# Kernel optimization log

Measured on AMD Instinct MI355X. Metric: run time of the kernel, lower is better.

The kernel has to match this reference:

```python
import jax, jax.numpy as jnp
import numpy as np

B, S, ENC = 64, 2048, 1024          # batch, encoder seq len, encoder feature dim
U, E_DIM, V_SZ = 512, 256, 50000    # dec_units, embedding_dim, vocab_size
IN_DIM = ENC + E_DIM                # LSTM input: [context ; token embedding]


def setup_inputs() -> dict:
    key = jax.random.key(0)
    ks = jax.random.split(key, 16)
    g = lambda k, shp, s=0.02: (jax.random.normal(k, shp, jnp.float32) * s)
    return {
        "x": jax.random.randint(ks[0], (B, 1), 0, V_SZ),
        "c_fwd": g(ks[1], (B, U), 0.1),
        "c_bwd": g(ks[2], (B, U), 0.1),
        "enc_output": jax.random.normal(ks[3], (B, S, ENC), jnp.float32),
        "emb": g(ks[4], (V_SZ, E_DIM)),
        "W1_w": g(ks[5], (ENC, U)), "W1_b": jnp.zeros((U,), jnp.float32),
        "W2_w": g(ks[6], (U, U)),   "W2_b": jnp.zeros((U,), jnp.float32),
        "W3_w": g(ks[7], (U, U)),   "W3_b": jnp.zeros((U,), jnp.float32),
        "V_w": g(ks[8], (U, 1)),    "V_b": jnp.zeros((1,), jnp.float32),
        "Kf": g(ks[9], (IN_DIM, 4 * U)),  "bf": jnp.zeros((4 * U,), jnp.float32),
        "Kb": g(ks[10], (IN_DIM, 4 * U)), "bb": jnp.zeros((4 * U,), jnp.float32),
        "fc_w": g(ks[11], (2 * U, V_SZ)), "fc_b": jnp.zeros((V_SZ,), jnp.float32),
    }


def _lstm_step_zero_state(xin, K, b):
    # Keras LSTM single step from zero (h0, c0): recurrent term vanishes.
    # Gate order in Keras kernel: i, f, c(g), o.
    z = xin @ K + b
    i, f, g, o = jnp.split(z, 4, axis=-1)
    i, o = jax.nn.sigmoid(i), jax.nn.sigmoid(o)  # f gate multiplies c0=0
    c = i * jnp.tanh(g)
    h = o * jnp.tanh(c)
    return h, c


def reference(x, c_fwd, c_bwd, enc_output, emb,
              W1_w, W1_b, W2_w, W2_b, W3_w, W3_b, V_w, V_b,
              Kf, bf, Kb, bb, fc_w, fc_b):
    # Bahdanau additive attention: score [B, S, 1]
    hidden_proj = (c_fwd @ W2_w + W2_b + c_bwd @ W3_w + W3_b)[:, None, :]  # [B,1,U]
    score = jnp.tanh(enc_output @ W1_w + W1_b + hidden_proj) @ V_w + V_b
    attn = jax.nn.softmax(score, axis=1)                 # softmax over S
    ctx = jnp.sum(attn * enc_output, axis=1)             # [B, ENC]

    xe = emb[x[:, 0]]                                    # [B, E_DIM]
    xin = jnp.concatenate([ctx, xe], axis=-1)            # [B, ENC+E_DIM]

    # Bidirectional LSTM over a length-1 sequence from zero initial state:
    # both directions see the same single timestep with separate weights.
    hf, cf = _lstm_step_zero_state(xin, Kf, bf)
    hb, cb = _lstm_step_zero_state(xin, Kb, bb)

    out = jnp.concatenate([hf, hb], axis=-1)             # [B, 2U]
    logits = out @ fc_w + fc_b                           # [B, vocab]
    return logits, hf, cf, hb, cb
```

## Files before the change

kernel.cpp:

```cpp
#include <hip/hip_runtime.h>

using u16 = unsigned short;
typedef float f32x4 __attribute__((ext_vector_type(4)));
typedef __bf16 bf16x8 __attribute__((ext_vector_type(8)));
typedef u16 u16x8 __attribute__((ext_vector_type(8)));

static constexpr int OF_HPB   = 262144;
static constexpr int OF_CTXP  = 294912;
static constexpr int OF_STATS = 2392064;
static constexpr int OF_XIN   = 2394112;
static constexpr int OF_ZPART = 2476032;
static constexpr size_t SCRATCH_FLOATS = 3000320;
static constexpr size_t SCRATCH_BYTES = SCRATCH_FLOATS * 4ull;

__device__ __forceinline__ u16 f2bf(float f) {
  unsigned u = __float_as_uint(f);
  u += 0x7FFFu + ((u >> 16) & 1u);
  return (u16)(u >> 16);
}
__device__ __forceinline__ float fast_tanh(float x) {
  x = fminf(fmaxf(x, -20.f), 20.f);
  float e = __expf(2.f * x);
  return (e - 1.f) / (e + 1.f);
}
__device__ __forceinline__ float fast_sig(float x) { return 1.f / (1.f + __expf(-x)); }

__global__ void k_prep_w1(const float* __restrict__ W1w, u16* __restrict__ w1p) {
  __shared__ float tile[32][132];
  const int t = threadIdx.x;
  const int ks = blockIdx.x >> 2, u0 = (blockIdx.x & 3) * 128;
  {
    int kk = t >> 3, ui = (t & 7) * 16;
    const float* src = W1w + (size_t)(ks * 32 + kk) * 512 + u0 + ui;
    #pragma unroll
    for (int i = 0; i < 4; ++i)
      *(float4*)&tile[kk][ui + i * 4] = *(const float4*)(src + i * 4);
  }
  __syncthreads();
  {
    int u = t >> 1, kh = (t & 1) * 16;
    u16x8 p0, p1;
    #pragma unroll
    for (int i = 0; i < 8; ++i) {
      p0[i] = f2bf(tile[kh + i][u]);
      p1[i] = f2bf(tile[kh + 8 + i][u]);
    }
    u16* dst = w1p + ((size_t)ks * 512 + u0 + u) * 32 + kh;
    *(u16x8*)(dst)     = p0;
    *(u16x8*)(dst + 8) = p1;
  }
}

__global__ void k_prep_hp(const float* __restrict__ cf, const float* __restrict__ cb,
                          const float* __restrict__ W2w, const float* __restrict__ W2b,
                          const float* __restrict__ W3w, const float* __restrict__ W3b,
                          const float* __restrict__ W1b, float* __restrict__ hpb) {
  __shared__ float cfl[512], cbl[512];
  const int b = blockIdx.x, t = threadIdx.x;
  cfl[t] = cf[(size_t)b * 512 + t];       cfl[t + 256] = cf[(size_t)b * 512 + t + 256];
  cbl[t] = cb[(size_t)b * 512 + t];       cbl[t + 256] = cb[(size_t)b * 512 + t + 256];
  __syncthreads();
  const int u1 = t, u2 = t + 256;
  float a1 = W2b[u1] + W3b[u1] + W1b[u1];
  float a2 = W2b[u2] + W3b[u2] + W1b[u2];
  for (int k = 0; k < 512; ++k) {
    float c1 = cfl[k], c2 = cbl[k];
    const float* r2 = W2w + (size_t)k * 512;
    const float* r3 = W3w + (size_t)k * 512;
    a1 += c1 * r2[u1] + c2 * r3[u1];
    a2 += c1 * r2[u2] + c2 * r3[u2];
  }
  hpb[(size_t)b * 512 + u1] = a1;
  hpb[(size_t)b * 512 + u2] = a2;
}

__global__ void __launch_bounds__(1024, 4)
k_attn(const float* __restrict__ enc, const u16* __restrict__ w1p,
       const float* __restrict__ hpb, const float* __restrict__ Vw,
       const float* __restrict__ Vb, float* __restrict__ ctxp,
       float* __restrict__ stats) {
  __shared__ u16 encA[65536];
  __shared__ float red[64][9];
  __shared__ float sc[64];
  __shared__ float pc[512][2];

  const int t = threadIdx.x;
  const int bid = blockIdx.x;
  const int b = bid >> 5, ch = bid & 31;
  const size_t rowbase = (size_t)b * 2048 + ch * 64;

  {
    const int r = t >> 4;
    const int cb = (t & 15) * 8;
    const int swz = (r & 7) << 3;
    const float* src = enc + (rowbase + r) * 1024 + cb;
    #pragma unroll
    for (int j = 0; j < 8; ++j) {
      float4 v0 = *(const float4*)(src + j * 128);
      float4 v1 = *(const float4*)(src + j * 128 + 4);
      u16x8 p;
      p[0]=f2bf(v0.x); p[1]=f2bf(v0.y); p[2]=f2bf(v0.z); p[3]=f2bf(v0.w);
      p[4]=f2bf(v1.x); p[5]=f2bf(v1.y); p[6]=f2bf(v1.z); p[7]=f2bf(v1.w);
      *(u16x8*)&encA[r * 1024 + ((cb + j * 128) ^ swz)] = p;
    }
  }
  __syncthreads();

  const int l = t & 63, w = t >> 6;
  const int wm = w >> 3, wn = w & 7;
  const int ln = l & 15, lg = l >> 4;

  f32x4 acc[2][4];
  #pragma unroll
  for (int im = 0; im < 2; ++im)
    #pragma unroll
    for (int nf = 0; nf < 4; ++nf)
      acc[im][nf] = f32x4{0.f, 0.f, 0.f, 0.f};

  const u16* bbase = w1p + (size_t)(wn * 64 + ln) * 32 + lg * 8;
  const int ar0 = wm * 32 + ln;
  const int aswz = (ln & 7) << 3;
  const u16* a0p = &encA[ar0 * 1024];
  const u16* a1p = &encA[(ar0 + 16) * 1024];

  u16x8 bcur[4], bnxt[4];
  #pragma unroll
  for (int nf = 0; nf < 4; ++nf)
    bcur[nf] = *(const u16x8*)(bbase + nf * 512);

  #pragma unroll 2
  for (int ks = 0; ks < 32; ++ks) {
    if (ks < 31) {
      const u16* bp = bbase + (size_t)(ks + 1) * 16384;
      #pragma unroll
      for (int nf = 0; nf < 4; ++nf)
        bnxt[nf] = *(const u16x8*)(bp + nf * 512);
    }
    const int ae = (ks * 32) ^ aswz;
    const int ofs = (ks * 32 + lg * 8) ^ aswz;
    bf16x8 a0 = *(const bf16x8*)(a0p + ofs);
    bf16x8 a1 = *(const bf16x8*)(a1p + ofs);
    (void)ae;
    #pragma unroll
    for (int nf = 0; nf < 4; ++nf) {
      bf16x8 bv = *(bf16x8*)&bcur[nf];
      acc[0][nf] = __builtin_amdgcn_mfma_f32_16x16x32_bf16(a0, bv, acc[0][nf], 0, 0, 0);
      acc[1][nf] = __builtin_amdgcn_mfma_f32_16x16x32_bf16(a1, bv, acc[1][nf], 0, 0, 0);
    }
    #pragma unroll
    for (int nf = 0; nf < 4; ++nf) bcur[nf] = bnxt[nf];
  }

  float vw_l[4], hp_l[4];
  #pragma unroll
  for (int nf = 0; nf < 4; ++nf) {
    int col = wn * 64 + nf * 16 + ln;
    vw_l[nf] = Vw[col];
    hp_l[nf] = hpb[(size_t)b * 512 + col];
  }
  #pragma unroll
  for (int im = 0; im < 2; ++im) {
    #pragma unroll
    for (int r = 0; r < 4; ++r) {
      float s = 0.f;
      #pragma unroll
      for (int nf = 0; nf < 4; ++nf)
        s += vw_l[nf] * fast_tanh(acc[im][nf][r] + hp_l[nf]);
      s += __shfl_xor(s, 1);
      s += __shfl_xor(s, 2);
      s += __shfl_xor(s, 4);
      s += __shfl_xor(s, 8);
      if (ln == 0) red[wm * 32 + im * 16 + lg * 4 + r][wn] = s;
    }
  }
  __syncthreads();
  if (t < 64) {
    float s = Vb[0];
    #pragma unroll
    for (int w2 = 0; w2 < 8; ++w2) s += red[t][w2];
    float e = __expf(s);
    sc[t] = e;
    float p = e;
    p += __shfl_xor(p, 1);  p += __shfl_xor(p, 2);  p += __shfl_xor(p, 4);
    p += __shfl_xor(p, 8);  p += __shfl_xor(p, 16); p += __shfl_xor(p, 32);
    if (t == 0) stats[bid] = p;
  }
  __syncthreads();

  {
    const int ci = (t & 511) * 2;
    const int r0 = (t >> 9) * 32;
    float a0 = 0.f, a1 = 0.f;
    for (int r = r0; r < r0 + 32; ++r) {
      unsigned v = *(const unsigned*)&encA[r * 1024 + (ci ^ ((r & 7) << 3))];
      float w0 = __uint_as_float(v << 16);
      float w1 = __uint_as_float(v & 0xFFFF0000u);
      a0 += sc[r] * w0;
      a1 += sc[r] * w1;
    }
    if (t >= 512) { pc[t - 512][0] = a0; pc[t - 512][1] = a1; }
    __syncthreads();
    if (t < 512) {
      float* dst = ctxp + (size_t)bid * 1024 + ci;
      dst[0] = a0 + pc[t][0];
      dst[1] = a1 + pc[t][1];
    }
  }
}

__global__ void k_attn_reduce(const float* __restrict__ ctxp, const float* __restrict__ stats,
                              const int* __restrict__ x, const float* __restrict__ emb,
                              float* __restrict__ xin) {
  __shared__ float ps[32];
  __shared__ float invs;
  const int b = blockIdx.x, t = threadIdx.x;
  if (t < 32) ps[t] = stats[b * 32 + t];
  __syncthreads();
  if (t == 0) {
    float s = 0.f;
    #pragma unroll
    for (int i = 0; i < 32; ++i) s += ps[i];
    invs = 1.f / s;
  }
  __syncthreads();
  const float inv = invs;
  #pragma unroll
  for (int i = 0; i < 4; ++i) {
    int c = t + i * 256;
    float a = 0.f;
    for (int chv = 0; chv < 32; ++chv)
      a += ctxp[((size_t)b * 32 + chv) * 1024 + c];
    xin[(size_t)b * 1280 + c] = a * inv;
  }
  xin[(size_t)b * 1280 + 1024 + t] = emb[(size_t)x[b] * 256 + t];
}

__global__ void k_lstm_gemm(const float* __restrict__ xin, const float* __restrict__ Kf,
                            const float* __restrict__ Kb, float* __restrict__ zpart) {
  __shared__ float xl[32][68];
  const int t = threadIdx.x;
  const int bid = blockIdx.x;
  const int dir = bid >> 7;
  const int jt  = (bid >> 1) & 63;
  const int ks  = bid & 1;
  const float* K = dir ? Kb : Kf;
  const int j  = jt * 32 + (t & 31);
  const int tb = t >> 5;
  const int brow = t >> 2, kq = (t & 3) * 8;
  float acc[8] = {0,0,0,0,0,0,0,0};
  for (int k0 = ks * 640; k0 < ks * 640 + 640; k0 += 32) {
    float4 x0 = *(const float4*)&xin[(size_t)brow * 1280 + k0 + kq];
    float4 x1 = *(const float4*)&xin[(size_t)brow * 1280 + k0 + kq + 4];
    __syncthreads();
    xl[kq+0][brow]=x0.x; xl[kq+1][brow]=x0.y; xl[kq+2][brow]=x0.z; xl[kq+3][brow]=x0.w;
    xl[kq+4][brow]=x1.x; xl[kq+5][brow]=x1.y; xl[kq+6][brow]=x1.z; xl[kq+7][brow]=x1.w;
    __syncthreads();
    const float* Kp = K + (size_t)k0 * 2048 + j;
    #pragma unroll 8
    for (int kk = 0; kk < 32; ++kk) {
      float wv = Kp[(size_t)kk * 2048];
      float4 v0 = *(const float4*)&xl[kk][tb * 8];
      float4 v1 = *(const float4*)&xl[kk][tb * 8 + 4];
      acc[0] += v0.x * wv; acc[1] += v0.y * wv; acc[2] += v0.z * wv; acc[3] += v0.w * wv;
      acc[4] += v1.x * wv; acc[5] += v1.y * wv; acc[6] += v1.z * wv; acc[7] += v1.w * wv;
    }
  }
  float* zp = zpart + ((size_t)dir * 2 + ks) * 64 * 2048;
  #pragma unroll
  for (int i = 0; i < 8; ++i)
    zp[(size_t)(tb * 8 + i) * 2048 + j] = acc[i];
}

__global__ void k_gates(const float* __restrict__ zpart, const float* __restrict__ bfv,
                        const float* __restrict__ bbv, float* __restrict__ dout) {
  const int dir = blockIdx.x >> 6, b = blockIdx.x & 63, u = threadIdx.x;
  const float* bias = dir ? bbv : bfv;
  const float* z0 = zpart + ((size_t)dir * 2 + 0) * 131072 + (size_t)b * 2048;
  const float* z1 = zpart + ((size_t)dir * 2 + 1) * 131072 + (size_t)b * 2048;
  float zi = z0[u]        + z1[u]        + bias[u];
  float zg = z0[1024 + u] + z1[1024 + u] + bias[1024 + u];
  float zo = z0[1536 + u] + z1[1536 + u] + bias[1536 + u];
  float c = fast_sig(zi) * fast_tanh(zg);
  float h = fast_sig(zo) * fast_tanh(c);
  size_t base = 3200000u + (size_t)dir * 65536u;
  dout[base + (size_t)b * 512 + u] = h;
  dout[base + 32768u + (size_t)b * 512 + u] = c;
}

__global__ void __launch_bounds__(256)
k_fc(const float* __restrict__ dout_ro, const float* __restrict__ fcw,
     const float* __restrict__ fcb, float* __restrict__ logits) {
  __shared__ float ol[64][68];
  __shared__ float wl[64][132];
  const int t = threadIdx.x;
  const int j0 = blockIdx.x * 128;
  const int tb = t >> 5, tj = t & 31;
  const float* hf = dout_ro + 3200000u;
  const float* hb = dout_ro + 3200000u + 65536u;
  float acc[8][4];
  #pragma unroll
  for (int bi = 0; bi < 8; ++bi)
    #pragma unroll
    for (int ji = 0; ji < 4; ++ji) acc[bi][ji] = 0.f;

  for (int k0 = 0; k0 < 1024; k0 += 64) {
    __syncthreads();
    {
      int bb = t >> 2, kq = (t & 3) * 16;
      const float* src = (k0 < 512) ? (hf + (size_t)bb * 512 + k0 + kq)
                                    : (hb + (size_t)bb * 512 + (k0 - 512) + kq);
      #pragma unroll
      for (int i = 0; i < 4; ++i) {
        float4 v = *(const float4*)(src + i * 4);
        ol[kq + i*4 + 0][bb] = v.x;
        ol[kq + i*4 + 1][bb] = v.y;
        ol[kq + i*4 + 2][bb] = v.z;
        ol[kq + i*4 + 3][bb] = v.w;
      }
    }
    {
      int kk = t >> 2, jh = (t & 3) * 32;
      const float* wsrc = fcw + (size_t)(k0 + kk) * 50000 + j0 + jh;
      #pragma unroll
      for (int i = 0; i < 8; ++i) {
        int j = j0 + jh + i * 4;
        float4 v;
        if (j + 3 < 50000) {
          v = *(const float4*)(wsrc + i * 4);
        } else {
          v.x = (j + 0 < 50000) ? wsrc[i*4 + 0] : 0.f;
          v.y = (j + 1 < 50000) ? wsrc[i*4 + 1] : 0.f;
          v.z = (j + 2 < 50000) ? wsrc[i*4 + 2] : 0.f;
          v.w = 0.f;
        }
        *(float4*)&wl[kk][jh + i * 4] = v;
      }
    }
    __syncthreads();
    #pragma unroll 4
    for (int kk = 0; kk < 64; ++kk) {
      float4 wv = *(const float4*)&wl[kk][tj * 4];
      float4 q0 = *(const float4*)&ol[kk][tb * 8];
      float4 q1 = *(const float4*)&ol[kk][tb * 8 + 4];
      float obv[8] = {q0.x, q0.y, q0.z, q0.w, q1.x, q1.y, q1.z, q1.w};
      #pragma unroll
      for (int bi = 0; bi < 8; ++bi) {
        acc[bi][0] += obv[bi] * wv.x;
        acc[bi][1] += obv[bi] * wv.y;
        acc[bi][2] += obv[bi] * wv.z;
        acc[bi][3] += obv[bi] * wv.w;
      }
    }
  }

  const int j = j0 + tj * 4;
  if (j + 3 < 50000) {
    float4 fb = *(const float4*)(fcb + j);
    #pragma unroll
    for (int bi = 0; bi < 8; ++bi) {
      float4 r;
      r.x = acc[bi][0] + fb.x; r.y = acc[bi][1] + fb.y;
      r.z = acc[bi][2] + fb.z; r.w = acc[bi][3] + fb.w;
      *(float4*)&logits[(size_t)(tb * 8 + bi) * 50000 + j] = r;
    }
  } else {
    for (int ji = 0; ji < 4; ++ji) {
      if (j + ji < 50000) {
        float fb = fcb[j + ji];
        for (int bi = 0; bi < 8; ++bi)
          logits[(size_t)(tb * 8 + bi) * 50000 + j + ji] = acc[bi][ji] + fb;
      }
    }
  }
}

extern "C" void kernel_launch(void* const* d_in, const int* in_sizes, int n_in,
                              void* d_out, int out_size, void* d_ws, size_t ws_size,
                              hipStream_t stream) {
  const int*   x    = (const int*)  d_in[0];
  const float* cfwd = (const float*)d_in[1];
  const float* cbwd = (const float*)d_in[2];
  const float* enc  = (const float*)d_in[3];
  const float* emb  = (const float*)d_in[4];
  const float* W1w  = (const float*)d_in[5];
  const float* W1b  = (const float*)d_in[6];
  const float* W2w  = (const float*)d_in[7];
  const float* W2b  = (const float*)d_in[8];
  const float* W3w  = (const float*)d_in[9];
  const float* W3b  = (const float*)d_in[10];
  const float* Vw   = (const float*)d_in[11];
  const float* Vb   = (const float*)d_in[12];
  const float* Kf   = (const float*)d_in[13];
  const float* bfv  = (const float*)d_in[14];
  const float* Kb   = (const float*)d_in[15];
  const float* bbv  = (const float*)d_in[16];
  const float* fcw  = (const float*)d_in[17];
  const float* fcb  = (const float*)d_in[18];
  float* out = (float*)d_out;

  float* S = (ws_size >= SCRATCH_BYTES) ? (float*)d_ws : out;
  u16*   w1p   = (u16*)S;
  float* hpb   = S + OF_HPB;
  float* ctxp  = S + OF_CTXP;
  float* stats = S + OF_STATS;
  float* xin   = S + OF_XIN;
  float* zpart = S + OF_ZPART;

  k_prep_w1<<<128, 256, 0, stream>>>(W1w, w1p);
  k_prep_hp<<<64, 256, 0, stream>>>(cfwd, cbwd, W2w, W2b, W3w, W3b, W1b, hpb);
  k_attn<<<2048, 1024, 0, stream>>>(enc, w1p, hpb, Vw, Vb, ctxp, stats);
  k_attn_reduce<<<64, 256, 0, stream>>>(ctxp, stats, x, emb, xin);
  k_lstm_gemm<<<256, 256, 0, stream>>>(xin, Kf, Kb, zpart);
  k_gates<<<128, 512, 0, stream>>>(zpart, bfv, bbv, out);
  k_fc<<<391, 256, 0, stream>>>(out, fcw, fcb, out);
}
```

Before: 633.3 us.

## Restructure attention GEMM with double-buffered LDS K-slices and async W1 loads

The attention kernel no longer converts the full 64x1024 encoder tile to bf16 in LDS up front. It streams 32-wide K slices of both the encoder tile and W1 into double-buffered LDS, using global_load_lds for W1, with 512 threads where each wave computes a 64x64 output tile. The context reduction now rereads the fp32 encoder rows from global memory with float4 loads instead of using the bf16 LDS copy, and LDS use drops from about 128KB to 80KB. The goal is to overlap loads with MFMA work and cut register and LDS pressure, at the cost of a second read of enc from global memory or cache and a barrier on every K step.

```diff
diff --git a/kernel.cpp b/kernel.cpp
--- a/kernel.cpp
+++ b/kernel.cpp
@@ -4,6 +4,7 @@
 typedef float f32x4 __attribute__((ext_vector_type(4)));
 typedef __bf16 bf16x8 __attribute__((ext_vector_type(8)));
 typedef u16 u16x8 __attribute__((ext_vector_type(8)));
+typedef u16 u16x4 __attribute__((ext_vector_type(4)));
 
 static constexpr int OF_HPB   = 262144;
 static constexpr int OF_CTXP  = 294912;
@@ -24,6 +25,12 @@
   return (e - 1.f) / (e + 1.f);
 }
 __device__ __forceinline__ float fast_sig(float x) { return 1.f / (1.f + __expf(-x)); }
+
+__device__ __forceinline__ void gll16(const u16* g, u16* l) {
+  __builtin_amdgcn_global_load_lds(
+      (const __attribute__((address_space(1))) unsigned int*)g,
+      (__attribute__((address_space(3))) unsigned int*)l, 16, 0, 0);
+}
 
 __global__ void k_prep_w1(const float* __restrict__ W1w, u16* __restrict__ w1p) {
   __shared__ float tile[32][132];
@@ -74,92 +81,91 @@
   hpb[(size_t)b * 512 + u2] = a2;
 }
 
-__global__ void __launch_bounds__(1024, 4)
+__global__ void __launch_bounds__(512, 4)
 k_attn(const float* __restrict__ enc, const u16* __restrict__ w1p,
        const float* __restrict__ hpb, const float* __restrict__ Vw,
        const float* __restrict__ Vb, float* __restrict__ ctxp,
        float* __restrict__ stats) {
-  __shared__ u16 encA[65536];
-  __shared__ float red[64][9];
-  __shared__ float sc[64];
-  __shared__ float pc[512][2];
+  __shared__ __align__(16) u16 smem[40960];
 
   const int t = threadIdx.x;
   const int bid = blockIdx.x;
-  const int b = bid >> 5, ch = bid & 31;
-  const size_t rowbase = (size_t)b * 2048 + ch * 64;
-
-  {
-    const int r = t >> 4;
-    const int cb = (t & 15) * 8;
-    const int swz = (r & 7) << 3;
-    const float* src = enc + (rowbase + r) * 1024 + cb;
-    #pragma unroll
-    for (int j = 0; j < 8; ++j) {
-      float4 v0 = *(const float4*)(src + j * 128);
-      float4 v1 = *(const float4*)(src + j * 128 + 4);
-      u16x8 p;
-      p[0]=f2bf(v0.x); p[1]=f2bf(v0.y); p[2]=f2bf(v0.z); p[3]=f2bf(v0.w);
-      p[4]=f2bf(v1.x); p[5]=f2bf(v1.y); p[6]=f2bf(v1.z); p[7]=f2bf(v1.w);
-      *(u16x8*)&encA[r * 1024 + ((cb + j * 128) ^ swz)] = p;
-    }
-  }
-  __syncthreads();
+  const int b = bid >> 5, tile = bid & 31;
+  const size_t row0 = (size_t)b * 2048 + (size_t)tile * 64;
 
   const int l = t & 63, w = t >> 6;
-  const int wm = w >> 3, wn = w & 7;
   const int ln = l & 15, lg = l >> 4;
 
-  f32x4 acc[2][4];
-  #pragma unroll
-  for (int im = 0; im < 2; ++im)
+  const int s_lg = (t >> 1) & 3, s_ln = (t >> 3) & 15, s_im = t >> 7, s_h = t & 1;
+  const float* a_src = enc + (row0 + s_im * 16 + s_ln) * 1024 + s_lg * 8 + s_h * 4;
+
+  f32x4 acc[4][4];
+  #pragma unroll
+  for (int im = 0; im < 4; ++im)
     #pragma unroll
     for (int nf = 0; nf < 4; ++nf)
       acc[im][nf] = f32x4{0.f, 0.f, 0.f, 0.f};
 
-  const u16* bbase = w1p + (size_t)(wn * 64 + ln) * 32 + lg * 8;
-  const int ar0 = wm * 32 + ln;
-  const int aswz = (ln & 7) << 3;
-  const u16* a0p = &encA[ar0 * 1024];
-  const u16* a1p = &encA[(ar0 + 16) * 1024];
-
-  u16x8 bcur[4], bnxt[4];
-  #pragma unroll
-  for (int nf = 0; nf < 4; ++nf)
-    bcur[nf] = *(const u16x8*)(bbase + nf * 512);
-
-  #pragma unroll 2
+  {
+    u16* Bn = smem;
+    #pragma unroll
+    for (int i = 0; i < 4; ++i)
+      gll16(w1p + i * 4096 + t * 8, Bn + i * 4096 + w * 512);
+    float4 av = *(const float4*)(a_src);
+    u16x4 aw4;
+    aw4[0] = f2bf(av.x); aw4[1] = f2bf(av.y); aw4[2] = f2bf(av.z); aw4[3] = f2bf(av.w);
+    *(u16x4*)(smem + 32768 + t * 4) = aw4;
+  }
+  __syncthreads();
+
   for (int ks = 0; ks < 32; ++ks) {
+    const int cur = ks & 1;
+    u16* Bc = smem + cur * 16384;
+    u16* Ac = smem + 32768 + cur * 4096;
+    float4 av;
     if (ks < 31) {
-      const u16* bp = bbase + (size_t)(ks + 1) * 16384;
+      u16* Bn = smem + (cur ^ 1) * 16384;
+      const u16* bsrc = w1p + (size_t)(ks + 1) * 16384 + t * 8;
+      #pragma unroll
+      for (int i = 0; i < 4; ++i)
+        gll16(bsrc + i * 4096, Bn + i * 4096 + w * 512);
+      av = *(const float4*)(a_src + (ks + 1) * 32);
+    }
+    bf16x8 afr[4], bfr[4];
+    #pragma unroll
+    for (int im = 0; im < 4; ++im)
+      afr[im] = *(const bf16x8*)(Ac + im * 512 + ln * 32 + lg * 8);
+    #pragma unroll
+    for (int nf = 0; nf < 4; ++nf)
+      bfr[nf] = *(const bf16x8*)(Bc + (w * 64 + nf * 16 + ln) * 32 + lg * 8);
+    #pragma unroll
+    for (int im = 0; im < 4; ++im)
       #pragma unroll
       for (int nf = 0; nf < 4; ++nf)
-        bnxt[nf] = *(const u16x8*)(bp + nf * 512);
-    }
-    const int ae = (ks * 32) ^ aswz;
-    const int ofs = (ks * 32 + lg * 8) ^ aswz;
-    bf16x8 a0 = *(const bf16x8*)(a0p + ofs);
-    bf16x8 a1 = *(const bf16x8*)(a1p + ofs);
-    (void)ae;
-    #pragma unroll
-    for (int nf = 0; nf < 4; ++nf) {
-      bf16x8 bv = *(bf16x8*)&bcur[nf];
-      acc[0][nf] = __builtin_amdgcn_mfma_f32_16x16x32_bf16(a0, bv, acc[0][nf], 0, 0, 0);
-      acc[1][nf] = __builtin_amdgcn_mfma_f32_16x16x32_bf16(a1, bv, acc[1][nf], 0, 0, 0);
-    }
-    #pragma unroll
-    for (int nf = 0; nf < 4; ++nf) bcur[nf] = bnxt[nf];
-  }
+        acc[im][nf] = __builtin_amdgcn_mfma_f32_16x16x32_bf16(afr[im], bfr[nf], acc[im][nf], 0, 0, 0);
+    if (ks < 31) {
+      u16* An = smem + 32768 + (cur ^ 1) * 4096;
+      u16x4 aw4;
+      aw4[0] = f2bf(av.x); aw4[1] = f2bf(av.y); aw4[2] = f2bf(av.z); aw4[3] = f2bf(av.w);
+      *(u16x4*)(An + t * 4) = aw4;
+    }
+    __syncthreads();
+  }
+
+  float* fsm = (float*)smem;
+  float* red = fsm;
+  float* scv = fsm + 576;
+  float* pcv = fsm + 640;
 
   float vw_l[4], hp_l[4];
   #pragma unroll
   for (int nf = 0; nf < 4; ++nf) {
-    int col = wn * 64 + nf * 16 + ln;
+    int col = w * 64 + nf * 16 + ln;
     vw_l[nf] = Vw[col];
     hp_l[nf] = hpb[(size_t)b * 512 + col];
   }
   #pragma unroll
-  for (int im = 0; im < 2; ++im) {
+  for (int im = 0; im < 4; ++im) {
     #pragma unroll
     for (int r = 0; r < 4; ++r) {
       float s = 0.f;
@@ -170,16 +176,16 @@
       s += __shfl_xor(s, 2);
       s += __shfl_xor(s, 4);
       s += __shfl_xor(s, 8);
-      if (ln == 0) red[wm * 32 + im * 16 + lg * 4 + r][wn] = s;
+      if (ln == 0) red[(im * 16 + lg * 4 + r) * 9 + w] = s;
     }
   }
   __syncthreads();
   if (t < 64) {
     float s = Vb[0];
     #pragma unroll
-    for (int w2 = 0; w2 < 8; ++w2) s += red[t][w2];
+    for (int w2 = 0; w2 < 8; ++w2) s += red[t * 9 + w2];
     float e = __expf(s);
-    sc[t] = e;
+    scv[t] = e;
     float p = e;
     p += __shfl_xor(p, 1);  p += __shfl_xor(p, 2);  p += __shfl_xor(p, 4);
     p += __shfl_xor(p, 8);  p += __shfl_xor(p, 16); p += __shfl_xor(p, 32);
@@ -188,22 +194,25 @@
   __syncthreads();
 
   {
-    const int ci = (t & 511) * 2;
-    const int r0 = (t >> 9) * 32;
-    float a0 = 0.f, a1 = 0.f;
-    for (int r = r0; r < r0 + 32; ++r) {
-      unsigned v = *(const unsigned*)&encA[r * 1024 + (ci ^ ((r & 7) << 3))];
-      float w0 = __uint_as_float(v << 16);
-      float w1 = __uint_as_float(v & 0xFFFF0000u);
-      a0 += sc[r] * w0;
-      a1 += sc[r] * w1;
-    }
-    if (t >= 512) { pc[t - 512][0] = a0; pc[t - 512][1] = a1; }
-    __syncthreads();
-    if (t < 512) {
-      float* dst = ctxp + (size_t)bid * 1024 + ci;
-      dst[0] = a0 + pc[t][0];
-      dst[1] = a1 + pc[t][1];
+    const int c4 = (t & 255) * 4;
+    const int rh = t >> 8;
+    const float* ep = enc + (row0 + rh * 32) * 1024 + c4;
+    float ax = 0.f, ay = 0.f, az = 0.f, aw2 = 0.f;
+    #pragma unroll 4
+    for (int r = 0; r < 32; ++r) {
+      float4 v = *(const float4*)(ep + (size_t)r * 1024);
+      float s = scv[rh * 32 + r];
+      ax += s * v.x; ay += s * v.y; az += s * v.z; aw2 += s * v.w;
+    }
+    if (t >= 256) {
+      float4 st = {ax, ay, az, aw2};
+      *(float4*)&pcv[c4] = st;
+    }
+    __syncthreads();
+    if (t < 256) {
+      float4 p2 = *(const float4*)&pcv[c4];
+      float4 o = {ax + p2.x, ay + p2.y, az + p2.z, aw2 + p2.w};
+      *(float4*)&ctxp[(size_t)bid * 1024 + c4] = o;
     }
   }
 }
@@ -408,7 +417,7 @@
 
   k_prep_w1<<<128, 256, 0, stream>>>(W1w, w1p);
   k_prep_hp<<<64, 256, 0, stream>>>(cfwd, cbwd, W2w, W2b, W3w, W3b, W1b, hpb);
-  k_attn<<<2048, 1024, 0, stream>>>(enc, w1p, hpb, Vw, Vb, ctxp, stats);
+  k_attn<<<2048, 512, 0, stream>>>(enc, w1p, hpb, Vw, Vb, ctxp, stats);
   k_attn_reduce<<<64, 256, 0, stream>>>(ctxp, stats, x, emb, xin);
   k_lstm_gemm<<<256, 256, 0, stream>>>(xin, Kf, Kb, zpart);
   k_gates<<<128, 512, 0, stream>>>(zpart, bfv, bbv, out);
```

After: 541.6 us. 1.17x faster.
